# Kernel optimization log

Hardware: AMD Instinct MI355X
Metric: run time of the kernel (lower is better)

The kernel has to match this reference:

```python
import jax, jax.numpy as jnp
import numpy as np

E, D, A, EMB, V = 2048, 512, 512, 512, 10000
B, HW, L = 64, 14, 52
P = HW * HW  # num_pixels
T = L - 1    # max decode length (we force max caption length == L)


def setup_inputs() -> dict:
    key = jax.random.key(0)
    ks = jax.random.split(key, 24)
    s = 0.02
    inp = {
        "encoder_out": jax.random.normal(ks[0], (B, HW, HW, E), jnp.float32),
        "encoded_captions": jax.random.randint(ks[1], (B, L), 0, V),
        "caption_lengths": jax.random.randint(ks[2], (B, 1), 2, L + 1).at[0, 0].set(L),
        # attention
        "W_ea": jax.random.normal(ks[3], (A, E)) * s, "b_ea": jnp.zeros((A,)),
        "W_da": jax.random.normal(ks[4], (A, D)) * s, "b_da": jnp.zeros((A,)),
        "w_fa": jax.random.normal(ks[5], (1, A)) * s, "b_fa": jnp.zeros((1,)),
        # embedding (uniform(-0.1,0.1) as in init_weights)
        "emb_table": jax.random.uniform(ks[6], (V, EMB), minval=-0.1, maxval=0.1),
        # LSTMCell: gates order i,f,g,o
        "W_ih": jax.random.normal(ks[7], (4 * D, EMB + E)) * s, "b_ih": jnp.zeros((4 * D,)),
        "W_hh": jax.random.normal(ks[8], (4 * D, D)) * s, "b_hh": jnp.zeros((4 * D,)),
        "W_init_h": jax.random.normal(ks[9], (D, E)) * s, "b_init_h": jnp.zeros((D,)),
        "W_init_c": jax.random.normal(ks[10], (D, E)) * s, "b_init_c": jnp.zeros((D,)),
        "W_fb": jax.random.normal(ks[11], (E, D)) * s, "b_fb": jnp.zeros((E,)),
        "W_fc": jax.random.uniform(ks[12], (V, D), minval=-0.1, maxval=0.1), "b_fc": jnp.zeros((V,)),
    }
    return inp


def _decode(encoder_out, encoded_captions, caption_lengths,
            W_ea, b_ea, W_da, b_da, w_fa, b_fa, emb_table,
            W_ih, b_ih, W_hh, b_hh, W_init_h, b_init_h,
            W_init_c, b_init_c, W_fb, b_fb, W_fc, b_fc):
    enc = encoder_out.reshape(B, -1, E)  # (B,P,E)
    lengths = caption_lengths[:, 0]
    order = jnp.argsort(-lengths)  # descending, stable
    lengths = lengths[order]
    enc = enc[order]
    caps = encoded_captions[order]
    dec_len = lengths - 1  # (B,)

    embeds = emb_table[caps]  # (B,L,EMB)
    mean_enc = enc.mean(axis=1)  # (B,E)
    h0 = mean_enc @ W_init_h.T + b_init_h
    c0 = mean_enc @ W_init_c.T + b_init_c

    # encoder side of attention is time-invariant; compute once
    att1 = jnp.einsum('bpe,ae->bpa', enc, W_ea) + b_ea  # (B,P,A)

    emb_seq = jnp.transpose(embeds[:, :T, :], (1, 0, 2))  # (T,B,EMB)
    ts = jnp.arange(T)

    def step(carry, xs):
        h, c = carry
        t, emb_t = xs
        mask = (t < dec_len)  # (B,)
        mf = mask[:, None].astype(h.dtype)
        # Bahdanau attention
        att2 = h @ W_da.T + b_da  # (B,A)
        e = jnp.einsum('bpa,a->bp', jax.nn.relu(att1 + att2[:, None, :]), w_fa[0]) + b_fa[0]
        alpha = jax.nn.softmax(e, axis=1)  # (B,P)
        awe = jnp.einsum('bpe,bp->be', enc, alpha)
        gate = jax.nn.sigmoid(h @ W_fb.T + b_fb)
        awe = gate * awe
        # LSTMCell
        x = jnp.concatenate([emb_t, awe], axis=1)  # (B, EMB+E)
        gates = x @ W_ih.T + b_ih + h @ W_hh.T + b_hh
        i_, f_, g_, o_ = jnp.split(gates, 4, axis=1)
        c2 = jax.nn.sigmoid(f_) * c + jax.nn.sigmoid(i_) * jnp.tanh(g_)
        h2 = jax.nn.sigmoid(o_) * jnp.tanh(c2)
        preds = h2 @ W_fc.T + b_fc  # dropout is identity in eval/reference
        h = jnp.where(mask[:, None], h2, h)
        c = jnp.where(mask[:, None], c2, c)
        return (h, c), (preds * mf, alpha * mf)

    (_, _), (preds_seq, alpha_seq) = jax.lax.scan(step, (h0, c0), (ts, emb_seq))
    predictions = jnp.transpose(preds_seq, (1, 0, 2))  # (B,T,V)
    alphas = jnp.transpose(alpha_seq, (1, 0, 2))       # (B,T,P)
    return predictions, caps, dec_len, alphas, order


def reference(encoder_out, encoded_captions, caption_lengths,
              W_ea, b_ea, W_da, b_da, w_fa, b_fa, emb_table,
              W_ih, b_ih, W_hh, b_hh, W_init_h, b_init_h,
              W_init_c, b_init_c, W_fb, b_fb, W_fc, b_fc):
    return _decode(encoder_out, encoded_captions, caption_lengths,
                   W_ea, b_ea, W_da, b_da, w_fa, b_fa, emb_table,
                   W_ih, b_ih, W_hh, b_hh, W_init_h, b_init_h,
                   W_init_c, b_init_c, W_fb, b_fb, W_fc, b_fc)
```

## Files before the change

### kernel.cpp

```cpp
#include <hip/hip_runtime.h>
#include <cmath>

#define NB 64
#define NP 196
#define NE 2048
#define NV 10000
#define NL 52
#define NT 51

typedef unsigned short bf16_t;
typedef __attribute__((ext_vector_type(8))) short bf16x8;
typedef __attribute__((ext_vector_type(4))) float f32x4;

__device__ inline unsigned short f2bf(float f){
  unsigned int x = __float_as_uint(f);
  unsigned int r = x + 0x7fffu + ((x>>16)&1u);
  return (unsigned short)(r>>16);
}
__device__ inline float bf2f(unsigned short u){ return __uint_as_float(((unsigned int)u)<<16); }
__device__ inline float sigm(float x){ return 1.f/(1.f+expf(-x)); }

__global__ void k_sort(const int* __restrict__ cap_len, const int* __restrict__ caps,
                       int* __restrict__ order, int* __restrict__ dlen, int* __restrict__ caps_s,
                       int* __restrict__ nact,
                       float* __restrict__ out_caps, float* __restrict__ out_dlen, float* __restrict__ out_order){
  __shared__ int len_s[NB];
  __shared__ int ord_s[NB];
  __shared__ int dls[NB];
  int t = threadIdx.x;
  len_s[t] = cap_len[t];
  __syncthreads();
  int li = len_s[t]; int rank = 0;
  for(int j=0;j<NB;j++){ int lj = len_s[j]; rank += ((lj > li) || (lj==li && j<t)) ? 1 : 0; }
  ord_s[rank] = t;
  __syncthreads();
  int ob = ord_s[t];
  order[t] = ob; out_order[t] = (float)ob;
  int ls = len_s[ob]; dlen[t] = ls-1; out_dlen[t] = (float)(ls-1); dls[t] = ls-1;
  for(int l=0;l<NL;l++){ int cv = caps[ob*NL + l]; caps_s[t*NL+l]=cv; out_caps[t*NL+l] = (float)cv; }
  __syncthreads();
  if(t < NT){
    int cnt=0;
    for(int b=0;b<NB;b++) cnt += (dls[b] > t) ? 1 : 0;
    nact[t] = cnt;
  }
}

__global__ __launch_bounds__(256) void k_cvt4(const float* __restrict__ src, bf16_t* __restrict__ dst, int n4){
  int i = blockIdx.x*blockDim.x + threadIdx.x;
  int stride = gridDim.x*blockDim.x;
  for(; i<n4; i+=stride){
    float4 v = ((const float4*)src)[i];
    unsigned long long p = (unsigned long long)f2bf(v.x)
        | ((unsigned long long)f2bf(v.y)<<16)
        | ((unsigned long long)f2bf(v.z)<<32)
        | ((unsigned long long)f2bf(v.w)<<48);
    ((unsigned long long*)dst)[i] = p;
  }
}

__global__ __launch_bounds__(256) void k_cvt2d4(const float* __restrict__ src, int rows, int cols,
                                                bf16_t* __restrict__ dst, int dld, int doff){
  int n4 = rows*cols/4;
  int c4n = cols/4;
  int i = blockIdx.x*blockDim.x + threadIdx.x;
  int stride = gridDim.x*blockDim.x;
  for(; i<n4; i+=stride){
    int r = i / c4n, c4 = i % c4n;
    float4 v = ((const float4*)src)[i];
    unsigned long long p = (unsigned long long)f2bf(v.x)
        | ((unsigned long long)f2bf(v.y)<<16)
        | ((unsigned long long)f2bf(v.z)<<32)
        | ((unsigned long long)f2bf(v.w)<<48);
    *(unsigned long long*)(dst + (size_t)r*dld + doff + c4*4) = p;
  }
}

__global__ __launch_bounds__(256) void k_mean(const float* __restrict__ enc, const int* __restrict__ order,
                                              bf16_t* __restrict__ me_s){
  int bs = blockIdx.x; int ec = blockIdx.y; int e = ec*256 + threadIdx.x;
  int ob = order[bs];
  const float* p = enc + (size_t)ob*NP*NE + e;
  float acc=0.f;
  for(int q=0;q<NP;q++) acc += p[(size_t)q*NE];
  me_s[(size_t)bs*NE + e] = f2bf(acc * (1.0f/NP));
}

__global__ __launch_bounds__(256) void k_emb(const int* __restrict__ caps_s, const float* __restrict__ emb_table,
                                             bf16_t* __restrict__ embAll){
  int b = blockIdx.x, t = blockIdx.y, tid = threadIdx.x;
  int cap = caps_s[b*NL + t];
  bf16_t* dst = embAll + ((size_t)t*NB + b)*512;
  const float* src = emb_table + (size_t)cap*512;
  dst[tid]       = f2bf(src[tid]);
  dst[tid + 256] = f2bf(src[tid + 256]);
}

template<int MODE>
__global__ __launch_bounds__(256) void k_big(const bf16_t* __restrict__ A, int lda, int Kdim,
      const bf16_t* __restrict__ Bw, int nrowsB,
      const float* __restrict__ bias, float* __restrict__ outf, bf16_t* __restrict__ outb,
      const int* __restrict__ dlen){
  __shared__ __align__(16) char smem_raw[36864];
  bf16_t (*As)[72] = (bf16_t(*)[72])smem_raw;
  bf16_t (*Bs)[72] = (bf16_t(*)[72])(smem_raw + 18432);
  int nblk = blockIdx.x, mblk = blockIdx.y;
  int tid = threadIdx.x;
  int w = tid>>6, l = tid&63;
  int moff = (w>>1)*64, noff = (w&1)*64;
  f32x4 acc[4][4] = {};
  const int mbase = mblk*128, nbase = nblk*128;
  for(int k0=0; k0<Kdim; k0+=64){
    __syncthreads();
    for(int u=0;u<4;u++){
      int lin = u*256 + tid; int row = lin>>3; int col = (lin&7)*8;
      *(bf16x8*)(&As[row][col]) = *(const bf16x8*)(A + (size_t)(mbase+row)*lda + k0 + col);
      int rB = nbase+row; if(MODE==2 && rB >= nrowsB) rB = nrowsB-1;
      *(bf16x8*)(&Bs[row][col]) = *(const bf16x8*)(Bw + (size_t)rB*lda + k0 + col);
    }
    __syncthreads();
    for(int kk=0;kk<2;kk++){
      bf16x8 af[4], bfr[4];
      for(int m=0;m<4;m++) af[m] = *(bf16x8*)(&As[moff + 16*m + (l&15)][kk*32 + (l>>4)*8]);
      for(int n=0;n<4;n++) bfr[n] = *(bf16x8*)(&Bs[noff + 16*n + (l&15)][kk*32 + (l>>4)*8]);
      for(int m=0;m<4;m++)
        for(int n=0;n<4;n++)
          acc[m][n] = __builtin_amdgcn_mfma_f32_16x16x32_bf16(af[m], bfr[n], acc[m][n], 0,0,0);
    }
  }
  if(MODE==0){
    for(int m=0;m<4;m++) for(int n=0;n<4;n++){
      int col = nbase + noff + 16*n + (l&15);
      float bi = bias[col];
      for(int r=0;r<4;r++){
        int row = mbase + moff + 16*m + (l>>4)*4 + r;
        outb[(size_t)row*512 + col] = f2bf(acc[m][n][r] + bi);
      }
    }
  } else {
    float* st = (float*)smem_raw;
    for(int h=0; h<2; ++h){
      __syncthreads();
      if((w>>1)==h){
        for(int m=0;m<4;m++) for(int n=0;n<4;n++)
          for(int r=0;r<4;r++)
            st[(16*m + (l>>4)*4 + r)*128 + noff + 16*n + (l&15)] = acc[m][n][r];
      }
      __syncthreads();
      for(int rr = tid>>5; rr<64; rr+=8){
        int row = mbase + h*64 + rr;
        if(row < NT*NB){
          int tt = row>>6, bb = row&63;
          int cc = (tid&31)*4;
          int col0 = nbase + cc;
          if(col0 < NV){
            float4 v = *(float4*)&st[rr*128 + cc];
            float4 bi4 = *(const float4*)&bias[col0];
            v.x+=bi4.x; v.y+=bi4.y; v.z+=bi4.z; v.w+=bi4.w;
            if(tt >= dlen[bb]){ v.x=0.f; v.y=0.f; v.z=0.f; v.w=0.f; }
            *(float4*)&outf[((size_t)bb*NT + tt)*NV + col0] = v;
          }
        }
      }
    }
  }
}

template<int KSL>
__global__ __launch_bounds__(256) void k_gemm_part(const bf16_t* __restrict__ Ax, int lda,
        const bf16_t* __restrict__ W, int ldw, float* __restrict__ part, int N){
  __shared__ bf16_t As[64][KSL+8];
  int ntile = blockIdx.x, ks = blockIdx.y;
  int tid = threadIdx.x; int w = tid>>6, l = tid&63;
  int k0 = ks*KSL;
  constexpr int UPR = KSL/8;
  constexpr int UPT = 64*UPR/256;
  for(int u=0;u<UPT;u++){
    int lin = u*256 + tid; int row = lin/UPR; int col = (lin%UPR)*8;
    *(bf16x8*)(&As[row][col]) = *(const bf16x8*)(Ax + (size_t)row*lda + k0 + col);
  }
  __syncthreads();
  f32x4 acc[4][4] = {};
  int nbase = ntile*256 + w*64;
  for(int kk=0; kk<KSL/32; kk++){
    bf16x8 af[4], bfr[4];
    for(int m=0;m<4;m++) af[m] = *(bf16x8*)(&As[16*m + (l&15)][kk*32 + (l>>4)*8]);
    for(int n=0;n<4;n++) bfr[n] = *(const bf16x8*)(W + (size_t)(nbase + 16*n + (l&15))*ldw + k0 + kk*32 + (l>>4)*8);
    for(int m=0;m<4;m++)
      for(int n=0;n<4;n++)
        acc[m][n] = __builtin_amdgcn_mfma_f32_16x16x32_bf16(af[m], bfr[n], acc[m][n], 0,0,0);
  }
  float* po = part + (size_t)ks*64*N;
  for(int m=0;m<4;m++) for(int n=0;n<4;n++){
    int col = nbase + 16*n + (l&15);
    for(int r=0;r<4;r++){
      int row = 16*m + (l>>4)*4 + r;
      po[(size_t)row*N + col] = acc[m][n][r];
    }
  }
}

__global__ __launch_bounds__(256) void k_init_fin(const float* __restrict__ part,
        const float* __restrict__ b_ih_, const float* __restrict__ b_ic_,
        float* __restrict__ c, bf16_t* __restrict__ h0){
  int idx = blockIdx.x*256 + threadIdx.x;
  int b_ = idx>>9, d = idx&511;
  float h = b_ih_[d], cc = b_ic_[d];
  for(int ks=0;ks<4;ks++){
    const float* p = part + (size_t)ks*64*1024 + (size_t)b_*1024;
    h += p[d]; cc += p[512+d];
  }
  c[idx] = cc;
  h0[(size_t)b_*512 + d] = f2bf(h);
}

__global__ __launch_bounds__(256) void k_e(const bf16_t* __restrict__ att1,
    const float* __restrict__ a2g, const float* __restrict__ b_da,
    const float* __restrict__ w_fa, const float* __restrict__ b_fa,
    const int* __restrict__ order, const int* __restrict__ nact,
    float* __restrict__ e_out, int t){
  int b_ = blockIdx.x, pg = blockIdx.y, tid = threadIdx.x;
  if(b_ >= nact[t]) return;
  int w = tid>>6, l = tid&63;
  int ob = order[b_];
  const float* pa0 = a2g + ((size_t)0*NB + b_)*2560;
  const float* pa1 = a2g + ((size_t)1*NB + b_)*2560;
  const float* pa2 = a2g + ((size_t)2*NB + b_)*2560;
  const float* pa3 = a2g + ((size_t)3*NB + b_)*2560;
  float ar[8], wr[8];
  #pragma unroll
  for(int q=0;q<8;q++){
    int i = l*8 + q;
    ar[q] = pa0[i] + pa1[i] + pa2[i] + pa3[i] + b_da[i];
    wr[q] = w_fa[i];
  }
  float bfa0 = b_fa[0];
  for(int pl=w; pl<49; pl+=4){
    int p = pg*49 + pl;
    bf16x8 a1v = *(const bf16x8*)(att1 + ((size_t)ob*NP + p)*512 + l*8);
    float s = 0.f;
    #pragma unroll
    for(int q=0;q<8;q++){
      float v = bf2f((unsigned short)a1v[q]) + ar[q];
      v = v>0.f ? v : 0.f;
      s += v*wr[q];
    }
    #pragma unroll
    for(int off=32;off;off>>=1) s += __shfl_down(s, off);
    if(l==0) e_out[b_*NP + p] = s + bfa0;
  }
}

__global__ __launch_bounds__(256) void k_awe(const bf16_t* __restrict__ enc, const float* __restrict__ e_in,
    const float* __restrict__ a2g, const float* __restrict__ b_fb,
    const int* __restrict__ order, const int* __restrict__ nact,
    float* __restrict__ alphas_out, bf16_t* __restrict__ xh_awe, int t){
  int b_ = blockIdx.x, y = blockIdx.y, tid = threadIdx.x;
  if(b_ >= nact[t]){
    if(y==0 && tid<NP) alphas_out[((size_t)b_*NT + t)*NP + tid] = 0.f;
    return;
  }
  __shared__ float al[200];
  __shared__ float red[8];
  __shared__ float aw[4][512];
  int w = tid>>6, l = tid&63;
  float v = (tid<NP)? e_in[b_*NP + tid] : -1e30f;
  float m = v;
  #pragma unroll
  for(int off=32;off;off>>=1) m = fmaxf(m, __shfl_down(m, off));
  if(l==0) red[w] = m;
  __syncthreads();
  float mx = fmaxf(fmaxf(red[0],red[1]), fmaxf(red[2],red[3]));
  float ex = (tid<NP)? expf(v - mx) : 0.f;
  float s2 = ex;
  #pragma unroll
  for(int off=32;off;off>>=1) s2 += __shfl_down(s2, off);
  if(l==0) red[4+w] = s2;
  __syncthreads();
  float inv = 1.f/(red[4]+red[5]+red[6]+red[7]);
  if(tid<NP){
    float a = ex*inv;
    al[tid] = a;
    if(y==0) alphas_out[((size_t)b_*NT + t)*NP + tid] = a;
  }
  __syncthreads();
  int ob = order[b_];
  int j0 = y*512 + l*8;
  float a8[8] = {};
  const bf16_t* ep = enc + (size_t)ob*NP*NE + j0;
  int p0 = w*49;
  #pragma unroll 4
  for(int pp=0; pp<49; ++pp){
    int p = p0 + pp;
    bf16x8 ev = *(const bf16x8*)(ep + (size_t)p*NE);
    float alp = al[p];
    #pragma unroll
    for(int q=0;q<8;q++) a8[q] += alp*bf2f((unsigned short)ev[q]);
  }
  #pragma unroll
  for(int q=0;q<8;q++) aw[w][l*8 + q] = a8[q];
  __syncthreads();
  const float* pa0 = a2g + ((size_t)0*NB + b_)*2560;
  const float* pa1 = a2g + ((size_t)1*NB + b_)*2560;
  const float* pa2 = a2g + ((size_t)2*NB + b_)*2560;
  const float* pa3 = a2g + ((size_t)3*NB + b_)*2560;
  int jl = tid*2;
  int j  = y*512 + jl;
  #pragma unroll
  for(int q=0;q<2;q++){
    float s = aw[0][jl+q] + aw[1][jl+q] + aw[2][jl+q] + aw[3][jl+q];
    int jj = 512 + j + q;
    float gpre = pa0[jj] + pa1[jj] + pa2[jj] + pa3[jj] + b_fb[j + q];
    xh_awe[(size_t)b_*2048 + j + q] = f2bf(sigm(gpre)*s);
  }
}

__global__ __launch_bounds__(256) void k_gatecell(const bf16_t* __restrict__ embT,
    const bf16_t* __restrict__ xh_awe, const bf16_t* __restrict__ hr,
    bf16_t* __restrict__ hw, const bf16_t* __restrict__ Wcat,
    const float* __restrict__ b_ih, const float* __restrict__ b_hh,
    float* __restrict__ cbuf, bf16_t* __restrict__ h2all,
    const int* __restrict__ dlen, int t){
  __shared__ float part[4][64][16];
  int j = blockIdx.x, tid = threadIdx.x;
  int w = tid>>6, l = tid&63;
  int n_ = l&15;
  int wrow = (n_>>2)*512 + j*4 + (n_&3);
  const bf16_t* wp = Wcat + (size_t)wrow*3072;
  f32x4 acc[4] = {};
  int k0w = w*768;
  for(int kk=0;kk<24;kk++){
    int col = k0w + kk*32 + (l>>4)*8;
    bf16x8 af[4], bg;
    if(col < 512){
      #pragma unroll
      for(int m=0;m<4;m++) af[m] = *(const bf16x8*)(embT + (size_t)(16*m + n_)*512 + col);
    } else if(col < 2560){
      #pragma unroll
      for(int m=0;m<4;m++) af[m] = *(const bf16x8*)(xh_awe + (size_t)(16*m + n_)*2048 + col - 512);
    } else {
      #pragma unroll
      for(int m=0;m<4;m++) af[m] = *(const bf16x8*)(hr + (size_t)(16*m + n_)*512 + col - 2560);
    }
    bg = *(const bf16x8*)(wp + col);
    #pragma unroll
    for(int m=0;m<4;m++)
      acc[m] = __builtin_amdgcn_mfma_f32_16x16x32_bf16(af[m], bg, acc[m], 0,0,0);
  }
  #pragma unroll
  for(int m=0;m<4;m++)
    #pragma unroll
    for(int r=0;r<4;r++)
      part[w][16*m + (l>>4)*4 + r][n_] = acc[m][r];
  __syncthreads();
  int b = tid>>2, c = tid&3;
  int dg = j*4 + c;
  float gs[4];
  #pragma unroll
  for(int g=0;g<4;g++){
    gs[g] = b_ih[g*512+dg] + b_hh[g*512+dg]
          + part[0][b][g*4+c] + part[1][b][g*4+c]
          + part[2][b][g*4+c] + part[3][b][g*4+c];
  }
  float oldc = cbuf[b*512 + dg];
  float c2 = sigm(gs[1])*oldc + sigm(gs[0])*tanhf(gs[2]);
  float h2 = sigm(gs[3])*tanhf(c2);
  bool mk = t < dlen[b];
  if(mk) cbuf[b*512 + dg] = c2;
  hw[(size_t)b*512 + dg] = mk ? f2bf(h2) : hr[(size_t)b*512 + dg];
  h2all[((size_t)t*NB + b)*512 + dg] = f2bf(h2);
}

extern "C" void kernel_launch(void* const* d_in, const int* in_sizes, int n_in,
                              void* d_out, int out_size, void* d_ws, size_t ws_size,
                              hipStream_t stream){
  (void)in_sizes; (void)n_in; (void)out_size; (void)ws_size;
  const float* encoder_out      = (const float*)d_in[0];
  const int*   encoded_captions = (const int*)d_in[1];
  const int*   caption_lengths  = (const int*)d_in[2];
  const float* W_ea = (const float*)d_in[3];  const float* b_ea = (const float*)d_in[4];
  const float* W_da = (const float*)d_in[5];  const float* b_da = (const float*)d_in[6];
  const float* w_fa = (const float*)d_in[7];  const float* b_fa = (const float*)d_in[8];
  const float* emb_table = (const float*)d_in[9];
  const float* W_ih = (const float*)d_in[10]; const float* b_ih = (const float*)d_in[11];
  const float* W_hh = (const float*)d_in[12]; const float* b_hh = (const float*)d_in[13];
  const float* W_init_h = (const float*)d_in[14]; const float* b_init_h = (const float*)d_in[15];
  const float* W_init_c = (const float*)d_in[16]; const float* b_init_c = (const float*)d_in[17];
  const float* W_fb = (const float*)d_in[18]; const float* b_fb = (const float*)d_in[19];
  const float* W_fc = (const float*)d_in[20]; const float* b_fc = (const float*)d_in[21];

  float* out_preds = (float*)d_out;
  float* out_caps  = out_preds + (size_t)NB*NT*NV;
  float* out_dlen  = out_caps + NB*NL;
  float* out_alph  = out_dlen + NB;
  float* out_order = out_alph + (size_t)NB*NT*NP;

  char* ws = (char*)d_ws;
  size_t off = 0;
  auto alloc = [&](size_t bytes)->size_t{ size_t r = off; off += (bytes + 255) & ~(size_t)255; return r; };
  bf16_t* enc_b   = (bf16_t*)(ws + alloc((size_t)12544*2048*2));
  char*   reg_att1 = ws + alloc((size_t)12544*512*2);
  bf16_t* att1_b  = (bf16_t*)reg_att1;
  float*  ipart   = (float*)reg_att1;
  char*   reg_h2   = ws + alloc((size_t)3328*512*2);
  bf16_t* h2all_b = (bf16_t*)reg_h2;
  bf16_t* Wea_b   = (bf16_t*)reg_h2;
  bf16_t* Wdafb_b = (bf16_t*)(ws + alloc((size_t)2560*512*2));
  bf16_t* Wcat_b  = (bf16_t*)(ws + alloc((size_t)2048*3072*2));
  bf16_t* Wfc_b   = (bf16_t*)(ws + alloc((size_t)10000*512*2));
  char*   reg_wi  = ws + alloc((size_t)1024*2048*2);
  bf16_t* Winit_b = (bf16_t*)reg_wi;
  bf16_t* embAll  = (bf16_t*)reg_wi;
  bf16_t* me_b    = (bf16_t*)(ws + alloc((size_t)64*2048*2));
  bf16_t* xh_awe  = (bf16_t*)(ws + alloc((size_t)64*2048*2));
  bf16_t* hbuf0   = (bf16_t*)(ws + alloc((size_t)64*512*2));
  bf16_t* hbuf1   = (bf16_t*)(ws + alloc((size_t)64*512*2));
  float*  c_f     = (float*)(ws + alloc((size_t)64*512*4));
  float*  a2gp_f  = (float*)(ws + alloc((size_t)4*64*2560*4));
  float*  e_f     = (float*)(ws + alloc((size_t)64*196*4));
  int*    order_i = (int*)(ws + alloc(64*4));
  int*    dlen_i  = (int*)(ws + alloc(64*4));
  int*    nact_i  = (int*)(ws + alloc(64*4));
  int*    caps_i  = (int*)(ws + alloc((size_t)64*52*4));

  k_sort<<<1,64,0,stream>>>(caption_lengths, encoded_captions, order_i, dlen_i, caps_i, nact_i,
                            out_caps, out_dlen, out_order);
  k_cvt4<<<2048,256,0,stream>>>(encoder_out, enc_b, 12544*2048/4);
  k_cvt4<<<512,256,0,stream>>>(W_ea, Wea_b, 512*2048/4);
  k_cvt4<<<256,256,0,stream>>>(W_da, Wdafb_b, 512*512/4);
  k_cvt4<<<512,256,0,stream>>>(W_fb, Wdafb_b + 512*512, 2048*512/4);
  k_cvt2d4<<<1024,256,0,stream>>>(W_ih, 2048, 2560, Wcat_b, 3072, 0);
  k_cvt2d4<<<512,256,0,stream>>>(W_hh, 2048, 512, Wcat_b, 3072, 2560);
  k_cvt4<<<512,256,0,stream>>>(W_init_h, Winit_b, 512*2048/4);
  k_cvt4<<<512,256,0,stream>>>(W_init_c, Winit_b + 512*2048, 512*2048/4);
  k_cvt4<<<1024,256,0,stream>>>(W_fc, Wfc_b, 10000*512/4);
  k_mean<<<dim3(64,8),256,0,stream>>>(encoder_out, order_i, me_b);
  k_gemm_part<512><<<dim3(4,4),256,0,stream>>>(me_b, 2048, Winit_b, 2048, ipart, 1024);
  k_init_fin<<<128,256,0,stream>>>(ipart, b_init_h, b_init_c, c_f, hbuf0);
  k_emb<<<dim3(NB,NT),256,0,stream>>>(caps_i, emb_table, embAll);
  k_big<0><<<dim3(4,98),256,0,stream>>>(enc_b, 2048, 2048, Wea_b, 512, b_ea, nullptr, att1_b, nullptr);
  k_gemm_part<128><<<dim3(10,4),256,0,stream>>>(hbuf0, 512, Wdafb_b, 512, a2gp_f, 2560);

  bf16_t* hb[2] = { hbuf0, hbuf1 };
  for(int t=0;t<NT;t++){
    bf16_t* hr = hb[t&1];
    bf16_t* hw = hb[(t&1)^1];
    k_e<<<dim3(64,4),256,0,stream>>>(att1_b, a2gp_f, b_da, w_fa, b_fa, order_i, nact_i, e_f, t);
    k_awe<<<dim3(64,4),256,0,stream>>>(enc_b, e_f, a2gp_f, b_fb, order_i, nact_i,
                                       out_alph, xh_awe, t);
    k_gatecell<<<128,256,0,stream>>>(embAll + (size_t)t*NB*512, xh_awe, hr, hw, Wcat_b,
                                     b_ih, b_hh, c_f, h2all_b, dlen_i, t);
    k_gemm_part<128><<<dim3(10,4),256,0,stream>>>(hw, 512, Wdafb_b, 512, a2gp_f, 2560);
  }
  k_big<2><<<dim3(79,26),256,0,stream>>>(h2all_b, 512, 512, Wfc_b, NV, b_fc, out_preds, nullptr, dlen_i);
}
```

Measured before the change: 2.696 ms.

## Fuse attention score and context kernels, split gate cell wider, remap big GEMM blocks per XCD

The attention score kernel and the softmax/weighted-encoder kernel are merged into one, so each block recomputes all 196 scores in shared memory instead of round-tripping them through global memory. The cost is that each of the 4 y-blocks per batch row now redundantly computes every score. The gate cell kernel now handles 2 hidden units per block across 256 blocks instead of 4 units across 128, for more parallelism at the price of half-wasted MFMA columns. The two large GEMMs switch to a 1D grid with an XCD-aware block remapping meant to improve L2 locality on the chiplet layout.

Measured after the change: 3.560 ms. +32.0%, slower.

```diff
diff --git a/kernel.cpp b/kernel.cpp
--- a/kernel.cpp
+++ b/kernel.cpp
@@ -104,7 +104,16 @@
   __shared__ __align__(16) char smem_raw[36864];
   bf16_t (*As)[72] = (bf16_t(*)[72])smem_raw;
   bf16_t (*Bs)[72] = (bf16_t(*)[72])(smem_raw + 18432);
-  int nblk = blockIdx.x, mblk = blockIdx.y;
+  int lid = blockIdx.x;
+  int nblk, mblk;
+  if(MODE==0){
+    int wg = (lid&7)*49 + (lid>>3);
+    mblk = wg>>2; nblk = wg&3;
+  } else {
+    int xcd = lid&7; int idx = lid>>3;
+    int wg = (xcd<6) ? xcd*257 + idx : 1542 + (xcd-6)*256 + idx;
+    nblk = wg/26; mblk = wg - nblk*26;
+  }
   int tid = threadIdx.x;
   int w = tid>>6, l = tid&63;
   int moff = (w>>1)*64, noff = (w&1)*64;
@@ -214,13 +223,20 @@
   h0[(size_t)b_*512 + d] = f2bf(h);
 }
 
-__global__ __launch_bounds__(256) void k_e(const bf16_t* __restrict__ att1,
-    const float* __restrict__ a2g, const float* __restrict__ b_da,
+__global__ __launch_bounds__(256) void k_attawe(const bf16_t* __restrict__ att1,
+    const bf16_t* __restrict__ enc,
+    const float* __restrict__ a2g, const float* __restrict__ b_da, const float* __restrict__ b_fb,
     const float* __restrict__ w_fa, const float* __restrict__ b_fa,
     const int* __restrict__ order, const int* __restrict__ nact,
-    float* __restrict__ e_out, int t){
-  int b_ = blockIdx.x, pg = blockIdx.y, tid = threadIdx.x;
-  if(b_ >= nact[t]) return;
+    float* __restrict__ alphas_out, bf16_t* __restrict__ xh_awe, int t){
+  int b_ = blockIdx.x, y = blockIdx.y, tid = threadIdx.x;
+  if(b_ >= nact[t]){
+    if(y==0 && tid<NP) alphas_out[((size_t)b_*NT + t)*NP + tid] = 0.f;
+    return;
+  }
+  __shared__ float al[200];
+  __shared__ float red[8];
+  __shared__ float aw[4][512];
   int w = tid>>6, l = tid&63;
   int ob = order[b_];
   const float* pa0 = a2g + ((size_t)0*NB + b_)*2560;
@@ -235,8 +251,7 @@
     wr[q] = w_fa[i];
   }
   float bfa0 = b_fa[0];
-  for(int pl=w; pl<49; pl+=4){
-    int p = pg*49 + pl;
+  for(int p=w; p<NP; p+=4){
     bf16x8 a1v = *(const bf16x8*)(att1 + ((size_t)ob*NP + p)*512 + l*8);
     float s = 0.f;
     #pragma unroll
@@ -247,24 +262,10 @@
     }
     #pragma unroll
     for(int off=32;off;off>>=1) s += __shfl_down(s, off);
-    if(l==0) e_out[b_*NP + p] = s + bfa0;
-  }
-}
-
-__global__ __launch_bounds__(256) void k_awe(const bf16_t* __restrict__ enc, const float* __restrict__ e_in,
-    const float* __restrict__ a2g, const float* __restrict__ b_fb,
-    const int* __restrict__ order, const int* __restrict__ nact,
-    float* __restrict__ alphas_out, bf16_t* __restrict__ xh_awe, int t){
-  int b_ = blockIdx.x, y = blockIdx.y, tid = threadIdx.x;
-  if(b_ >= nact[t]){
-    if(y==0 && tid<NP) alphas_out[((size_t)b_*NT + t)*NP + tid] = 0.f;
-    return;
-  }
-  __shared__ float al[200];
-  __shared__ float red[8];
-  __shared__ float aw[4][512];
-  int w = tid>>6, l = tid&63;
-  float v = (tid<NP)? e_in[b_*NP + tid] : -1e30f;
+    if(l==0) al[p] = s + bfa0;
+  }
+  __syncthreads();
+  float v = (tid<NP)? al[tid] : -1e30f;
   float m = v;
   #pragma unroll
   for(int off=32;off;off>>=1) m = fmaxf(m, __shfl_down(m, off));
@@ -278,13 +279,13 @@
   if(l==0) red[4+w] = s2;
   __syncthreads();
   float inv = 1.f/(red[4]+red[5]+red[6]+red[7]);
+  __syncthreads();
   if(tid<NP){
     float a = ex*inv;
     al[tid] = a;
     if(y==0) alphas_out[((size_t)b_*NT + t)*NP + tid] = a;
   }
   __syncthreads();
-  int ob = order[b_];
   int j0 = y*512 + l*8;
   float a8[8] = {};
   const bf16_t* ep = enc + (size_t)ob*NP*NE + j0;
@@ -300,10 +301,6 @@
   #pragma unroll
   for(int q=0;q<8;q++) aw[w][l*8 + q] = a8[q];
   __syncthreads();
-  const float* pa0 = a2g + ((size_t)0*NB + b_)*2560;
-  const float* pa1 = a2g + ((size_t)1*NB + b_)*2560;
-  const float* pa2 = a2g + ((size_t)2*NB + b_)*2560;
-  const float* pa3 = a2g + ((size_t)3*NB + b_)*2560;
   int jl = tid*2;
   int j  = y*512 + jl;
   #pragma unroll
@@ -321,11 +318,12 @@
     const float* __restrict__ b_ih, const float* __restrict__ b_hh,
     float* __restrict__ cbuf, bf16_t* __restrict__ h2all,
     const int* __restrict__ dlen, int t){
-  __shared__ float part[4][64][16];
+  __shared__ float part[4][64][8];
   int j = blockIdx.x, tid = threadIdx.x;
   int w = tid>>6, l = tid&63;
   int n_ = l&15;
-  int wrow = (n_>>2)*512 + j*4 + (n_&3);
+  int rowsel = n_&7;
+  int wrow = (rowsel>>1)*512 + j*2 + (rowsel&1);
   const bf16_t* wp = Wcat + (size_t)wrow*3072;
   f32x4 acc[4] = {};
   int k0w = w*768;
@@ -347,28 +345,32 @@
     for(int m=0;m<4;m++)
       acc[m] = __builtin_amdgcn_mfma_f32_16x16x32_bf16(af[m], bg, acc[m], 0,0,0);
   }
-  #pragma unroll
-  for(int m=0;m<4;m++)
-    #pragma unroll
-    for(int r=0;r<4;r++)
-      part[w][16*m + (l>>4)*4 + r][n_] = acc[m][r];
-  __syncthreads();
-  int b = tid>>2, c = tid&3;
-  int dg = j*4 + c;
-  float gs[4];
-  #pragma unroll
-  for(int g=0;g<4;g++){
-    gs[g] = b_ih[g*512+dg] + b_hh[g*512+dg]
-          + part[0][b][g*4+c] + part[1][b][g*4+c]
-          + part[2][b][g*4+c] + part[3][b][g*4+c];
-  }
-  float oldc = cbuf[b*512 + dg];
-  float c2 = sigm(gs[1])*oldc + sigm(gs[0])*tanhf(gs[2]);
-  float h2 = sigm(gs[3])*tanhf(c2);
-  bool mk = t < dlen[b];
-  if(mk) cbuf[b*512 + dg] = c2;
-  hw[(size_t)b*512 + dg] = mk ? f2bf(h2) : hr[(size_t)b*512 + dg];
-  h2all[((size_t)t*NB + b)*512 + dg] = f2bf(h2);
+  if(n_ < 8){
+    #pragma unroll
+    for(int m=0;m<4;m++)
+      #pragma unroll
+      for(int r=0;r<4;r++)
+        part[w][16*m + (l>>4)*4 + r][n_] = acc[m][r];
+  }
+  __syncthreads();
+  if(tid < 128){
+    int b = tid>>1, cc = tid&1;
+    int dg = j*2 + cc;
+    float gs[4];
+    #pragma unroll
+    for(int g=0;g<4;g++){
+      gs[g] = b_ih[g*512+dg] + b_hh[g*512+dg]
+            + part[0][b][g*2+cc] + part[1][b][g*2+cc]
+            + part[2][b][g*2+cc] + part[3][b][g*2+cc];
+    }
+    float oldc = cbuf[b*512 + dg];
+    float c2 = sigm(gs[1])*oldc + sigm(gs[0])*tanhf(gs[2]);
+    float h2 = sigm(gs[3])*tanhf(c2);
+    bool mk = t < dlen[b];
+    if(mk) cbuf[b*512 + dg] = c2;
+    hw[(size_t)b*512 + dg] = mk ? f2bf(h2) : hr[(size_t)b*512 + dg];
+    h2all[((size_t)t*NB + b)*512 + dg] = f2bf(h2);
+  }
 }
 
 extern "C" void kernel_launch(void* const* d_in, const int* in_sizes, int n_in,
@@ -417,7 +419,6 @@
   bf16_t* hbuf1   = (bf16_t*)(ws + alloc((size_t)64*512*2));
   float*  c_f     = (float*)(ws + alloc((size_t)64*512*4));
   float*  a2gp_f  = (float*)(ws + alloc((size_t)4*64*2560*4));
-  float*  e_f     = (float*)(ws + alloc((size_t)64*196*4));
   int*    order_i = (int*)(ws + alloc(64*4));
   int*    dlen_i  = (int*)(ws + alloc(64*4));
   int*    nact_i  = (int*)(ws + alloc(64*4));
@@ -438,19 +439,18 @@
   k_gemm_part<512><<<dim3(4,4),256,0,stream>>>(me_b, 2048, Winit_b, 2048, ipart, 1024);
   k_init_fin<<<128,256,0,stream>>>(ipart, b_init_h, b_init_c, c_f, hbuf0);
   k_emb<<<dim3(NB,NT),256,0,stream>>>(caps_i, emb_table, embAll);
-  k_big<0><<<dim3(4,98),256,0,stream>>>(enc_b, 2048, 2048, Wea_b, 512, b_ea, nullptr, att1_b, nullptr);
+  k_big<0><<<392,256,0,stream>>>(enc_b, 2048, 2048, Wea_b, 512, b_ea, nullptr, att1_b, nullptr);
   k_gemm_part<128><<<dim3(10,4),256,0,stream>>>(hbuf0, 512, Wdafb_b, 512, a2gp_f, 2560);
 
   bf16_t* hb[2] = { hbuf0, hbuf1 };
   for(int t=0;t<NT;t++){
     bf16_t* hr = hb[t&1];
     bf16_t* hw = hb[(t&1)^1];
-    k_e<<<dim3(64,4),256,0,stream>>>(att1_b, a2gp_f, b_da, w_fa, b_fa, order_i, nact_i, e_f, t);
-    k_awe<<<dim3(64,4),256,0,stream>>>(enc_b, e_f, a2gp_f, b_fb, order_i, nact_i,
-                                       out_alph, xh_awe, t);
-    k_gatecell<<<128,256,0,stream>>>(embAll + (size_t)t*NB*512, xh_awe, hr, hw, Wcat_b,
+    k_attawe<<<dim3(64,4),256,0,stream>>>(att1_b, enc_b, a2gp_f, b_da, b_fb, w_fa, b_fa,
+                                          order_i, nact_i, out_alph, xh_awe, t);
+    k_gatecell<<<256,256,0,stream>>>(embAll + (size_t)t*NB*512, xh_awe, hr, hw, Wcat_b,
                                      b_ih, b_hh, c_f, h2all_b, dlen_i, t);
     k_gemm_part<128><<<dim3(10,4),256,0,stream>>>(hw, 512, Wdafb_b, 512, a2gp_f, 2560);
   }
-  k_big<2><<<dim3(79,26),256,0,stream>>>(h2all_b, 512, 512, Wfc_b, NV, b_fc, out_preds, nullptr, dlen_i);
-}
+  k_big<2><<<2054,256,0,stream>>>(h2all_b, 512, 512, Wfc_b, NV, b_fc, out_preds, nullptr, dlen_i);
+}
```

## Batch weight conversions into one kernel, mean from bf16, XCD-aware GEMM block mapping

Applied to the files above, without the earlier changes.

Replaces eight separate weight-conversion launches with a single multi-region conversion kernel that takes a struct of pointers. The encoder mean now reads the already-converted bf16 encoder instead of re-reading the fp32 input, which halves that read traffic but computes the mean from rounded values. The two big GEMMs switch to 1D grids with a remapping of block IDs so that neighbouring tiles land on the same XCD, aiming for better L2 reuse of shared operand tiles. These are mostly one-time setup costs outside the 51-step decode loop, which likely dominates the runtime.

Result: no change. 2.672 ms (-0.9%).

```diff
diff --git a/kernel.cpp b/kernel.cpp
--- a/kernel.cpp
+++ b/kernel.cpp
@@ -59,30 +59,39 @@
   }
 }
 
-__global__ __launch_bounds__(256) void k_cvt2d4(const float* __restrict__ src, int rows, int cols,
-                                                bf16_t* __restrict__ dst, int dld, int doff){
-  int n4 = rows*cols/4;
-  int c4n = cols/4;
-  int i = blockIdx.x*blockDim.x + threadIdx.x;
+struct CvtRegs {
+  const float* src[8];
+  bf16_t* dst[8];
+  int start[9];
+  int cols4[8];
+  int dld[8];
+};
+
+__global__ __launch_bounds__(256) void k_cvtw(CvtRegs R, int total4){
+  int gid = blockIdx.x*blockDim.x + threadIdx.x;
   int stride = gridDim.x*blockDim.x;
-  for(; i<n4; i+=stride){
-    int r = i / c4n, c4 = i % c4n;
-    float4 v = ((const float4*)src)[i];
+  for(; gid<total4; gid+=stride){
+    int rgn = 0;
+    while(gid >= R.start[rgn+1]) rgn++;
+    int i = gid - R.start[rgn];
+    int c4n = R.cols4[rgn];
+    int r = i / c4n, c4 = i - r*c4n;
+    float4 v = ((const float4*)R.src[rgn])[i];
     unsigned long long p = (unsigned long long)f2bf(v.x)
         | ((unsigned long long)f2bf(v.y)<<16)
         | ((unsigned long long)f2bf(v.z)<<32)
         | ((unsigned long long)f2bf(v.w)<<48);
-    *(unsigned long long*)(dst + (size_t)r*dld + doff + c4*4) = p;
-  }
-}
-
-__global__ __launch_bounds__(256) void k_mean(const float* __restrict__ enc, const int* __restrict__ order,
+    *(unsigned long long*)(R.dst[rgn] + (size_t)r*R.dld[rgn] + c4*4) = p;
+  }
+}
+
+__global__ __launch_bounds__(256) void k_mean(const bf16_t* __restrict__ encb, const int* __restrict__ order,
                                               bf16_t* __restrict__ me_s){
   int bs = blockIdx.x; int ec = blockIdx.y; int e = ec*256 + threadIdx.x;
   int ob = order[bs];
-  const float* p = enc + (size_t)ob*NP*NE + e;
+  const bf16_t* p = encb + (size_t)ob*NP*NE + e;
   float acc=0.f;
-  for(int q=0;q<NP;q++) acc += p[(size_t)q*NE];
+  for(int q=0;q<NP;q++) acc += bf2f(p[(size_t)q*NE]);
   me_s[(size_t)bs*NE + e] = f2bf(acc * (1.0f/NP));
 }
 
@@ -104,7 +113,16 @@
   __shared__ __align__(16) char smem_raw[36864];
   bf16_t (*As)[72] = (bf16_t(*)[72])smem_raw;
   bf16_t (*Bs)[72] = (bf16_t(*)[72])(smem_raw + 18432);
-  int nblk = blockIdx.x, mblk = blockIdx.y;
+  int lid = blockIdx.x;
+  int nblk, mblk;
+  if(MODE==0){
+    int wg = (lid&7)*49 + (lid>>3);
+    mblk = wg>>2; nblk = wg&3;
+  } else {
+    int xcd = lid&7; int idx = lid>>3;
+    int wg = (xcd<6) ? xcd*257 + idx : 1542 + (xcd-6)*256 + idx;
+    nblk = wg/26; mblk = wg - nblk*26;
+  }
   int tid = threadIdx.x;
   int w = tid>>6, l = tid&63;
   int moff = (w>>1)*64, noff = (w&1)*64;
@@ -426,19 +444,26 @@
   k_sort<<<1,64,0,stream>>>(caption_lengths, encoded_captions, order_i, dlen_i, caps_i, nact_i,
                             out_caps, out_dlen, out_order);
   k_cvt4<<<2048,256,0,stream>>>(encoder_out, enc_b, 12544*2048/4);
-  k_cvt4<<<512,256,0,stream>>>(W_ea, Wea_b, 512*2048/4);
-  k_cvt4<<<256,256,0,stream>>>(W_da, Wdafb_b, 512*512/4);
-  k_cvt4<<<512,256,0,stream>>>(W_fb, Wdafb_b + 512*512, 2048*512/4);
-  k_cvt2d4<<<1024,256,0,stream>>>(W_ih, 2048, 2560, Wcat_b, 3072, 0);
-  k_cvt2d4<<<512,256,0,stream>>>(W_hh, 2048, 512, Wcat_b, 3072, 2560);
-  k_cvt4<<<512,256,0,stream>>>(W_init_h, Winit_b, 512*2048/4);
-  k_cvt4<<<512,256,0,stream>>>(W_init_c, Winit_b + 512*2048, 512*2048/4);
-  k_cvt4<<<1024,256,0,stream>>>(W_fc, Wfc_b, 10000*512/4);
-  k_mean<<<dim3(64,8),256,0,stream>>>(encoder_out, order_i, me_b);
+
+  CvtRegs R;
+  int n4s[8];
+  R.src[0] = W_ea;      R.dst[0] = Wea_b;               n4s[0] = 512*2048/4;  R.cols4[0] = 512; R.dld[0] = 2048;
+  R.src[1] = W_da;      R.dst[1] = Wdafb_b;             n4s[1] = 512*512/4;   R.cols4[1] = 128; R.dld[1] = 512;
+  R.src[2] = W_fb;      R.dst[2] = Wdafb_b + 512*512;   n4s[2] = 2048*512/4;  R.cols4[2] = 128; R.dld[2] = 512;
+  R.src[3] = W_ih;      R.dst[3] = Wcat_b;              n4s[3] = 2048*2560/4; R.cols4[3] = 640; R.dld[3] = 3072;
+  R.src[4] = W_hh;      R.dst[4] = Wcat_b + 2560;       n4s[4] = 2048*512/4;  R.cols4[4] = 128; R.dld[4] = 3072;
+  R.src[5] = W_init_h;  R.dst[5] = Winit_b;             n4s[5] = 512*2048/4;  R.cols4[5] = 512; R.dld[5] = 2048;
+  R.src[6] = W_init_c;  R.dst[6] = Winit_b + 512*2048;  n4s[6] = 512*2048/4;  R.cols4[6] = 512; R.dld[6] = 2048;
+  R.src[7] = W_fc;      R.dst[7] = Wfc_b;               n4s[7] = 10000*512/4; R.cols4[7] = 128; R.dld[7] = 512;
+  R.start[0] = 0;
+  for(int i=0;i<8;i++) R.start[i+1] = R.start[i] + n4s[i];
+  k_cvtw<<<1024,256,0,stream>>>(R, R.start[8]);
+
+  k_mean<<<dim3(64,8),256,0,stream>>>(enc_b, order_i, me_b);
   k_gemm_part<512><<<dim3(4,4),256,0,stream>>>(me_b, 2048, Winit_b, 2048, ipart, 1024);
   k_init_fin<<<128,256,0,stream>>>(ipart, b_init_h, b_init_c, c_f, hbuf0);
   k_emb<<<dim3(NB,NT),256,0,stream>>>(caps_i, emb_table, embAll);
-  k_big<0><<<dim3(4,98),256,0,stream>>>(enc_b, 2048, 2048, Wea_b, 512, b_ea, nullptr, att1_b, nullptr);
+  k_big<0><<<392,256,0,stream>>>(enc_b, 2048, 2048, Wea_b, 512, b_ea, nullptr, att1_b, nullptr);
   k_gemm_part<128><<<dim3(10,4),256,0,stream>>>(hbuf0, 512, Wdafb_b, 512, a2gp_f, 2560);
 
   bf16_t* hb[2] = { hbuf0, hbuf1 };
@@ -452,5 +477,5 @@
                                      b_ih, b_hh, c_f, h2all_b, dlen_i, t);
     k_gemm_part<128><<<dim3(10,4),256,0,stream>>>(hw, 512, Wdafb_b, 512, a2gp_f, 2560);
   }
-  k_big<2><<<dim3(79,26),256,0,stream>>>(h2all_b, 512, 512, Wfc_b, NV, b_fc, out_preds, nullptr, dlen_i);
-}
+  k_big<2><<<2054,256,0,stream>>>(h2all_b, 512, 512, Wfc_b, NV, b_fc, out_preds, nullptr, dlen_i);
+}
```
